# Optimization experiments

Measured on AMD Instinct MI355X. Metric: run time of the kernel, lower is better.

The kernel has to match this reference:

```python
import jax, jax.numpy as jnp
import numpy as np
from jax.scipy.linalg import cho_solve

N = 4096        # num nodes
D = 256         # in_dim == out_dim
NUM_HOPS = 2
R = 32          # subspace_dim
ETA = 0.5
EPS_SUB = 0.5   # eps in coeff = r / (n * eps^2)
LN_EPS = 1e-5


def setup_inputs() -> dict:
    rng = np.random.default_rng(0)
    K = NUM_HOPS + 1
    # sparse-ish binary adjacency mask with self loops
    mask = (rng.random((N, N)) < 0.002).astype(np.float32)
    mask = np.maximum(mask, np.eye(N, dtype=np.float32))
    deg = mask.sum(axis=1, keepdims=True)
    A = (mask / deg).astype(np.float32)          # row-stochastic propagation
    L = (np.eye(N, dtype=np.float32) - A)        # normalized Laplacian
    H = rng.standard_normal((N, D)).astype(np.float32)
    # orthonormal subspace bases per hop, as in __init__ (QR of randn)
    U = np.stack([np.linalg.qr(rng.standard_normal((D, R)))[0][:, :R] for _ in range(K)]).astype(np.float32)
    lambda_laps = np.full((K,), 0.1, dtype=np.float32)
    hop_weights = np.full((K,), 1.0 / K, dtype=np.float32)
    threshold = np.full((D,), 0.05, dtype=np.float32)
    gamma = np.ones((D,), dtype=np.float32)
    beta = np.zeros((D,), dtype=np.float32)
    return {
        "H": jnp.asarray(H), "A": jnp.asarray(A), "adj_mask": jnp.asarray(mask),
        "L": jnp.asarray(L), "U": jnp.asarray(U),
        "lambda_laps": jnp.asarray(lambda_laps), "hop_weights": jnp.asarray(hop_weights),
        "threshold": jnp.asarray(threshold), "gamma": jnp.asarray(gamma), "beta": jnp.asarray(beta),
    }


def reference(H, A, adj_mask, L, U, lambda_laps, hop_weights, threshold, gamma, beta):
    n, d = H.shape
    r = U.shape[-1]
    # multi-hop propagation
    hops = [H]
    Hk = H
    for _ in range(NUM_HOPS):
        Hk = A @ Hk
        hops.append(Hk)
    w = jax.nn.softmax(hop_weights)
    laps = jax.nn.softplus(lambda_laps)
    coeff = r / (n * EPS_SUB ** 2)
    neg = (1.0 - adj_mask) * -1e9
    I_r = jnp.eye(r, dtype=H.dtype)
    agg = jnp.zeros_like(H)        # accumulates grad_k.T, shape [n, d]
    lap_total = jnp.zeros_like(H)
    for k, H_k in enumerate(hops):
        Uk = U[k]                  # [d, r]
        Zk = Uk.T @ H_k.T          # [r, n]
        M = I_r + coeff * (Zk @ Zk.T)              # [r, r], SPD
        Lc = jnp.linalg.cholesky(M)
        M_inv = cho_solve((Lc, True), I_r)         # cholesky_inverse
        MZ = M_inv @ Zk                            # [r, n]
        scores = Zk.T @ MZ + neg                   # [n, n] masked subspace attention
        alpha = jax.nn.softmax(scores, axis=1)
        grad_k = (Uk @ (MZ @ alpha.T)).T           # [n, d]
        agg = agg + w[k] * grad_k
        lap_total = lap_total + laps[k] * (L @ H_k)
    H_half = H + ETA * agg - ETA * lap_total
    # soft-threshold (proj is None since in_dim == out_dim)
    H_out = jnp.sign(H_half) * jax.nn.relu(jnp.abs(H_half) - threshold[None, :])
    H_out = H_out + H              # residual
    mu = H_out.mean(axis=-1, keepdims=True)
    var = H_out.var(axis=-1, keepdims=True)
    H_out = (H_out - mu) / jnp.sqrt(var + LN_EPS) * gamma + beta
    # orthogonality loss over all (k, l) pairs
    K = U.shape[0]
    orth_loss = jnp.asarray(0.0, dtype=H.dtype)
    for k in range(K):
        for l in range(k, K):
            G = U[k].T @ U[l]
            orth_loss = orth_loss + jnp.sum(((G - I_r) if l == k else G) ** 2)
    lap_smooth = jnp.sum(H_out * (L @ H_out))  # trace(H^T L H)
    return H_out, orth_loss, lap_smooth, jax.lax.stop_gradient(w)
```

## Files before the change

### kernel.cpp

```cpp
#include <hip/hip_runtime.h>
#include <math.h>

#define NN 4096
#define DD 256
#define KK 3
#define RR 32
#define MAXNNZ 128

static constexpr float ETA    = 0.5f;
static constexpr float COEFF  = 0.03125f;
static constexpr float LN_EPSF = 1e-5f;

#define OFF_H1   0
#define OFF_H2   (NN*DD)
#define OFF_H3   (2*NN*DD)
#define OFF_Y    (3*NN*DD)
#define OFF_W    (OFF_Y + KK*NN*RR)
#define OFF_P    (OFF_W + KK*NN*RR)
#define OFF_M    (OFF_P + KK*NN*RR)
#define OFF_MINV (OFF_M + KK*RR*RR)
#define OFF_SCAL (OFF_MINV + KK*RR*RR)
#define OFF_NNZ  (OFF_SCAL + 8)
#define OFF_COLS (OFF_NNZ + NN)
#define OFF_VALS (OFF_COLS + NN*MAXNNZ)
#define OFF_PART (OFF_VALS + NN*MAXNNZ)

__global__ void k_prep(const float* __restrict__ hw, const float* __restrict__ ll,
                       float* __restrict__ ws, float* __restrict__ out) {
  int t = threadIdx.x;
  if (t == 0) {
    float m = fmaxf(fmaxf(hw[0], hw[1]), hw[2]);
    float e0 = expf(hw[0]-m), e1 = expf(hw[1]-m), e2 = expf(hw[2]-m);
    float s = e0 + e1 + e2;
    float w0 = e0/s, w1 = e1/s, w2 = e2/s;
    ws[OFF_SCAL+0] = w0; ws[OFF_SCAL+1] = w1; ws[OFF_SCAL+2] = w2;
    for (int k = 0; k < KK; ++k) {
      float x = ll[k];
      ws[OFF_SCAL+3+k] = (x > 20.f) ? x : log1pf(expf(x));
    }
    out[NN*DD + 0] = 0.f;
    out[NN*DD + 2] = w0; out[NN*DD + 3] = w1; out[NN*DD + 4] = w2;
  }
  for (int idx = t; idx < KK*RR*RR; idx += blockDim.x) {
    int rr2 = idx % (RR*RR);
    ws[OFF_M + idx] = ((rr2 / RR) == (rr2 % RR)) ? 1.f : 0.f;
  }
}

__global__ void k_csr(const float* __restrict__ A, int* __restrict__ nnz,
                      int* __restrict__ cols, float* __restrict__ vals) {
  int i = blockIdx.x;
  __shared__ int cnt;
  if (threadIdx.x == 0) cnt = 0;
  __syncthreads();
  const float4* row4 = (const float4*)(A + (size_t)i * NN);
  for (int j0 = 0; j0 < NN/4; j0 += 256) {
    float4 v = row4[j0 + threadIdx.x];
    int jb = (j0 + threadIdx.x) * 4;
    if (v.x != 0.f) { int p = atomicAdd(&cnt,1); if (p<MAXNNZ){cols[i*MAXNNZ+p]=jb+0; vals[i*MAXNNZ+p]=v.x;} }
    if (v.y != 0.f) { int p = atomicAdd(&cnt,1); if (p<MAXNNZ){cols[i*MAXNNZ+p]=jb+1; vals[i*MAXNNZ+p]=v.y;} }
    if (v.z != 0.f) { int p = atomicAdd(&cnt,1); if (p<MAXNNZ){cols[i*MAXNNZ+p]=jb+2; vals[i*MAXNNZ+p]=v.z;} }
    if (v.w != 0.f) { int p = atomicAdd(&cnt,1); if (p<MAXNNZ){cols[i*MAXNNZ+p]=jb+3; vals[i*MAXNNZ+p]=v.w;} }
  }
  __syncthreads();
  int n = cnt < MAXNNZ ? cnt : MAXNNZ;
  int npad = (n + 7) & ~7;
  for (int e = n + threadIdx.x; e < npad; e += 256) {
    cols[i*MAXNNZ + e] = i;
    vals[i*MAXNNZ + e] = 0.f;
  }
  if (threadIdx.x == 0) nnz[i] = n;
}

__global__ void k_spmv(const float* __restrict__ X, float* __restrict__ Y,
                       const int* __restrict__ nnz, const int* __restrict__ cols,
                       const float* __restrict__ vals) {
  int t = threadIdx.x;
  int row = blockIdx.x * 4 + (t >> 6);
  int d4 = (t & 63) * 4;
  int n = nnz[row];
  int npad = (n + 7) & ~7;
  const int* ci = cols + row*MAXNNZ;
  const float* vi = vals + row*MAXNNZ;
  float4 acc = {0.f, 0.f, 0.f, 0.f};
  for (int e0 = 0; e0 < npad; e0 += 8) {
    int4 c0 = *(const int4*)(ci + e0);
    int4 c1 = *(const int4*)(ci + e0 + 4);
    float4 v0 = *(const float4*)(vi + e0);
    float4 v1 = *(const float4*)(vi + e0 + 4);
    float4 x0 = *(const float4*)(X + (size_t)c0.x*DD + d4);
    float4 x1 = *(const float4*)(X + (size_t)c0.y*DD + d4);
    float4 x2 = *(const float4*)(X + (size_t)c0.z*DD + d4);
    float4 x3 = *(const float4*)(X + (size_t)c0.w*DD + d4);
    float4 x4 = *(const float4*)(X + (size_t)c1.x*DD + d4);
    float4 x5 = *(const float4*)(X + (size_t)c1.y*DD + d4);
    float4 x6 = *(const float4*)(X + (size_t)c1.z*DD + d4);
    float4 x7 = *(const float4*)(X + (size_t)c1.w*DD + d4);
    acc.x += v0.x*x0.x + v0.y*x1.x + v0.z*x2.x + v0.w*x3.x + v1.x*x4.x + v1.y*x5.x + v1.z*x6.x + v1.w*x7.x;
    acc.y += v0.x*x0.y + v0.y*x1.y + v0.z*x2.y + v0.w*x3.y + v1.x*x4.y + v1.y*x5.y + v1.z*x6.y + v1.w*x7.y;
    acc.z += v0.x*x0.z + v0.y*x1.z + v0.z*x2.z + v0.w*x3.z + v1.x*x4.z + v1.y*x5.z + v1.z*x6.z + v1.w*x7.z;
    acc.w += v0.x*x0.w + v0.y*x1.w + v0.z*x2.w + v0.w*x3.w + v1.x*x4.w + v1.y*x5.w + v1.z*x6.w + v1.w*x7.w;
  }
  *(float4*)(Y + (size_t)row*DD + d4) = acc;
}

__global__ void k_yproj(const float* __restrict__ H0, const float* __restrict__ Hws,
                        const float* __restrict__ U, float* __restrict__ Y) {
  int k = blockIdx.y;
  const float* Hk = (k == 0) ? H0 : (Hws + (size_t)(k-1)*NN*DD);
  __shared__ float Us[DD*RR];
  __shared__ float Hs[8][DD];
  int t = threadIdx.x;
  for (int idx = t; idx < DD*RR; idx += 256) Us[idx] = U[(size_t)k*DD*RR + idx];
  int row0 = blockIdx.x * 8;
  for (int r = 0; r < 8; ++r) Hs[r][t] = Hk[(size_t)(row0+r)*DD + t];
  __syncthreads();
  int rl = t >> 5, c = t & 31;
  const float4* H4 = (const float4*)Hs[rl];
  float acc = 0.f;
  for (int dd4 = 0; dd4 < DD/4; ++dd4) {
    float4 hv = H4[dd4];
    int b = dd4 * 4 * RR + c;
    acc += hv.x*Us[b] + hv.y*Us[b+RR] + hv.z*Us[b+2*RR] + hv.w*Us[b+3*RR];
  }
  Y[(size_t)k*NN*RR + (size_t)(row0+rl)*RR + c] = acc;
}

__global__ __launch_bounds__(1024) void k_gram(const float* __restrict__ Y, float* __restrict__ M) {
  int k = blockIdx.y;
  __shared__ float Ys[128*RR];
  int t = threadIdx.x;
  const float* Yk = Y + (size_t)k*NN*RR + (size_t)blockIdx.x*128*RR;
  for (int idx = t; idx < 128*RR; idx += 1024) Ys[idx] = Yk[idx];
  __syncthreads();
  int a = t >> 5, b = t & 31;
  float s = 0.f;
  for (int i = 0; i < 128; ++i) s += Ys[i*RR + a] * Ys[i*RR + b];
  atomicAdd(&M[k*RR*RR + a*RR + b], COEFF * s);
}

__global__ __launch_bounds__(1024) void k_cholinv(const float* __restrict__ M, float* __restrict__ Minv) {
  int k = blockIdx.x;
  __shared__ float L[RR][RR+1];
  __shared__ float Li[RR][RR+1];
  int t = threadIdx.x;
  int r = t >> 5, c = t & 31;
  L[r][c] = M[k*RR*RR + r*RR + c];
  Li[r][c] = 0.f;
  __syncthreads();
  for (int j = 0; j < RR; ++j) {
    if (t == j*32 + j) L[j][j] = sqrtf(L[j][j]);
    __syncthreads();
    if (c == j && r > j) L[r][j] /= L[j][j];
    __syncthreads();
    if (r > j && c > j && c <= r) L[r][c] -= L[r][j] * L[c][j];
    __syncthreads();
  }
  if (t < RR) {
    int cc = t;
    Li[cc][cc] = 1.f / L[cc][cc];
    for (int rr2 = cc+1; rr2 < RR; ++rr2) {
      float s = 0.f;
      for (int j = cc; j < rr2; ++j) s += L[rr2][j] * Li[j][cc];
      Li[rr2][cc] = -s / L[rr2][rr2];
    }
  }
  __syncthreads();
  float s = 0.f;
  int j0 = (r > c) ? r : c;
  for (int j = j0; j < RR; ++j) s += Li[j][r] * Li[j][c];
  Minv[k*RR*RR + r*RR + c] = s;
}

__global__ void k_wproj(const float* __restrict__ Y, const float* __restrict__ Minv,
                        float* __restrict__ W) {
  int k = blockIdx.y;
  __shared__ float Ms[RR*RR];
  __shared__ float Ys[8*RR];
  int t = threadIdx.x;
  for (int idx = t; idx < RR*RR; idx += 256) Ms[idx] = Minv[k*RR*RR + idx];
  int row0 = blockIdx.x * 8;
  Ys[t] = Y[(size_t)k*NN*RR + (size_t)row0*RR + t];
  __syncthreads();
  int rl = t >> 5, c = t & 31;
  float acc = 0.f;
  for (int a = 0; a < RR; ++a) acc += Ys[rl*RR + a] * Ms[a*RR + c];
  W[(size_t)k*NN*RR + (size_t)(row0+rl)*RR + c] = acc;
}

__global__ void k_attn(const float* __restrict__ Y, const float* __restrict__ W,
                       float* __restrict__ P, const int* __restrict__ nnz,
                       const int* __restrict__ cols) {
  int i = blockIdx.x;
  int t = threadIdx.x;
  int half = t >> 5, lane = t & 31;
  int n = nnz[i];
  int npad = (n + 7) & ~7;
  const int* ci = cols + i*MAXNNZ;
  __shared__ float sc[MAXNNZ];
  __shared__ float outp[2][RR];
  for (int k = 0; k < KK; ++k) {
    const float* Yk = Y + (size_t)k*NN*RR;
    const float* Wk = W + (size_t)k*NN*RR;
    float yv = Yk[(size_t)i*RR + lane];
    for (int e0 = 0; e0 < npad; e0 += 8) {
      #pragma unroll
      for (int u = 0; u < 4; ++u) {
        int e = e0 + 2*u + half;
        float p = yv * Wk[(size_t)ci[e]*RR + lane];
        #pragma unroll
        for (int o = 16; o > 0; o >>= 1) p += __shfl_down(p, o, 32);
        if (lane == 0) sc[e] = (e < n) ? p : -1e30f;
      }
    }
    __syncthreads();
    float s0 = (t < npad) ? sc[t] : -1e30f;
    float s1 = (t+64 < npad) ? sc[t+64] : -1e30f;
    float m = fmaxf(s0, s1);
    #pragma unroll
    for (int o = 32; o > 0; o >>= 1) m = fmaxf(m, __shfl_xor(m, o, 64));
    float ev0 = (t < npad) ? expf(s0 - m) : 0.f;
    float ev1 = (t+64 < npad) ? expf(s1 - m) : 0.f;
    if (t < npad) sc[t] = ev0;
    if (t+64 < npad) sc[t+64] = ev1;
    float l = ev0 + ev1;
    #pragma unroll
    for (int o = 32; o > 0; o >>= 1) l += __shfl_xor(l, o, 64);
    float linv = 1.f / l;
    __syncthreads();
    float acc = 0.f;
    for (int e0 = 0; e0 < npad; e0 += 8) {
      #pragma unroll
      for (int u = 0; u < 4; ++u) {
        int e = e0 + 2*u + half;
        acc += sc[e] * Wk[(size_t)ci[e]*RR + lane];
      }
    }
    outp[half][lane] = acc;
    __syncthreads();
    if (t < RR) P[(size_t)k*NN*RR + (size_t)i*RR + t] = (outp[0][t] + outp[1][t]) * linv;
    __syncthreads();
  }
}

__global__ void k_epi(const float* __restrict__ H0, const float* __restrict__ ws,
                      const float* __restrict__ U, const float* __restrict__ thr,
                      const float* __restrict__ gma, const float* __restrict__ bta,
                      float* __restrict__ out) {
  __shared__ float Us[DD][RR+1];
  __shared__ float Ps[8][KK*RR];
  int t = threadIdx.x;
  int ty = t >> 5, tx = t & 31;
  int row0 = blockIdx.x * 8;
  const float* P    = ws + OFF_P;
  const float* scal = ws + OFF_SCAL;
  for (int idx = t; idx < 8*KK*RR; idx += 256) {
    int rl = idx / (KK*RR), kr = idx % (KK*RR);
    int k = kr / RR, rr2 = kr % RR;
    Ps[rl][kr] = P[(size_t)k*NN*RR + (size_t)(row0+rl)*RR + rr2];
  }
  float lp0 = scal[3], lp1 = scal[4], lp2 = scal[5];
  float gacc[8];
  #pragma unroll
  for (int j = 0; j < 8; ++j) gacc[j] = 0.f;
  for (int k = 0; k < KK; ++k) {
    __syncthreads();
    for (int idx = t; idx < DD*RR; idx += 256) Us[idx >> 5][idx & 31] = U[(size_t)k*DD*RR + idx];
    __syncthreads();
    float wk = scal[k];
    #pragma unroll
    for (int j = 0; j < 8; ++j) {
      int d = tx + 32*j;
      float s = 0.f;
      #pragma unroll
      for (int rr2 = 0; rr2 < RR; ++rr2) s += Ps[ty][k*RR + rr2] * Us[d][rr2];
      gacc[j] += wk * s;
    }
  }
  int i = row0 + ty;
  const float* H1 = ws + OFF_H1;
  const float* H2 = ws + OFF_H2;
  const float* H3 = ws + OFF_H3;
  float v[8]; float sum = 0.f, sumsq = 0.f;
  #pragma unroll
  for (int j = 0; j < 8; ++j) {
    int d = tx + 32*j;
    size_t idx = (size_t)i*DD + d;
    float h0 = H0[idx], h1 = H1[idx], h2 = H2[idx], h3 = H3[idx];
    float lap = lp0*(h0-h1) + lp1*(h1-h2) + lp2*(h2-h3);
    float hf = h0 + ETA*gacc[j] - ETA*lap;
    float a = fabsf(hf) - thr[d];
    float sft = (a > 0.f) ? copysignf(a, hf) : 0.f;
    float x = sft + h0;
    v[j] = x; sum += x; sumsq += x*x;
  }
  #pragma unroll
  for (int o = 16; o > 0; o >>= 1) {
    sum   += __shfl_xor(sum, o, 32);
    sumsq += __shfl_xor(sumsq, o, 32);
  }
  float mu  = sum * (1.f/DD);
  float var = sumsq * (1.f/DD) - mu*mu;
  float inv = rsqrtf(var + LN_EPSF);
  #pragma unroll
  for (int j = 0; j < 8; ++j) {
    int d = tx + 32*j;
    out[(size_t)i*DD + d] = (v[j] - mu) * inv * gma[d] + bta[d];
  }
}

__global__ void k_lapsm(const float* __restrict__ Hout, const int* __restrict__ nnz,
                        const int* __restrict__ cols, const float* __restrict__ vals,
                        float* __restrict__ partial) {
  int t = threadIdx.x;
  int row = blockIdx.x * 4 + (t >> 6);
  int d4 = (t & 63) * 4;
  int n = nnz[row];
  int npad = (n + 7) & ~7;
  const int* ci = cols + row*MAXNNZ;
  const float* vi = vals + row*MAXNNZ;
  float4 acc = {0.f, 0.f, 0.f, 0.f};
  for (int e0 = 0; e0 < npad; e0 += 8) {
    int4 c0 = *(const int4*)(ci + e0);
    int4 c1 = *(const int4*)(ci + e0 + 4);
    float4 v0 = *(const float4*)(vi + e0);
    float4 v1 = *(const float4*)(vi + e0 + 4);
    float4 x0 = *(const float4*)(Hout + (size_t)c0.x*DD + d4);
    float4 x1 = *(const float4*)(Hout + (size_t)c0.y*DD + d4);
    float4 x2 = *(const float4*)(Hout + (size_t)c0.z*DD + d4);
    float4 x3 = *(const float4*)(Hout + (size_t)c0.w*DD + d4);
    float4 x4 = *(const float4*)(Hout + (size_t)c1.x*DD + d4);
    float4 x5 = *(const float4*)(Hout + (size_t)c1.y*DD + d4);
    float4 x6 = *(const float4*)(Hout + (size_t)c1.z*DD + d4);
    float4 x7 = *(const float4*)(Hout + (size_t)c1.w*DD + d4);
    acc.x += v0.x*x0.x + v0.y*x1.x + v0.z*x2.x + v0.w*x3.x + v1.x*x4.x + v1.y*x5.x + v1.z*x6.x + v1.w*x7.x;
    acc.y += v0.x*x0.y + v0.y*x1.y + v0.z*x2.y + v0.w*x3.y + v1.x*x4.y + v1.y*x5.y + v1.z*x6.y + v1.w*x7.y;
    acc.z += v0.x*x0.z + v0.y*x1.z + v0.z*x2.z + v0.w*x3.z + v1.x*x4.z + v1.y*x5.z + v1.z*x6.z + v1.w*x7.z;
    acc.w += v0.x*x0.w + v0.y*x1.w + v0.z*x2.w + v0.w*x3.w + v1.x*x4.w + v1.y*x5.w + v1.z*x6.w + v1.w*x7.w;
  }
  float4 h = *(const float4*)(Hout + (size_t)row*DD + d4);
  float part = h.x*(h.x-acc.x) + h.y*(h.y-acc.y) + h.z*(h.z-acc.z) + h.w*(h.w-acc.w);
  #pragma unroll
  for (int o = 32; o > 0; o >>= 1) part += __shfl_xor(part, o, 64);
  __shared__ float red[4];
  if ((t & 63) == 0) red[t >> 6] = part;
  __syncthreads();
  if (t == 0) partial[blockIdx.x] = red[0] + red[1] + red[2] + red[3];
}

__global__ void k_red(const float* __restrict__ partial, float* __restrict__ out) {
  int t = threadIdx.x;
  float4 p = *(const float4*)(partial + t*4);
  float s = p.x + p.y + p.z + p.w;
  #pragma unroll
  for (int o = 32; o > 0; o >>= 1) s += __shfl_xor(s, o, 64);
  __shared__ float red[4];
  if ((t & 63) == 0) red[t >> 6] = s;
  __syncthreads();
  if (t == 0) out[0] = red[0] + red[1] + red[2] + red[3];
}

__global__ __launch_bounds__(1024) void k_orth(const float* __restrict__ U, float* __restrict__ out) {
  int p = blockIdx.x;
  int k = (p < 3) ? 0 : ((p < 5) ? 1 : 2);
  int l = (p < 3) ? p : ((p < 5) ? p - 2 : 2);
  int t = threadIdx.x;
  int a = t >> 5, b = t & 31;
  float s = 0.f;
  for (int dd = 0; dd < DD; ++dd)
    s += U[(size_t)k*DD*RR + dd*RR + a] * U[(size_t)l*DD*RR + dd*RR + b];
  if (k == l && a == b) s -= 1.f;
  float sq = s * s;
  __shared__ float red[1024];
  red[t] = sq;
  __syncthreads();
  for (int st = 512; st > 0; st >>= 1) {
    if (t < st) red[t] += red[t + st];
    __syncthreads();
  }
  if (t == 0) atomicAdd(out, red[0]);
}

extern "C" void kernel_launch(void* const* d_in, const int* in_sizes, int n_in,
                              void* d_out, int out_size, void* d_ws, size_t ws_size,
                              hipStream_t stream) {
  const float* H   = (const float*)d_in[0];
  const float* A   = (const float*)d_in[1];
  const float* U   = (const float*)d_in[4];
  const float* ll  = (const float*)d_in[5];
  const float* hw  = (const float*)d_in[6];
  const float* thr = (const float*)d_in[7];
  const float* gma = (const float*)d_in[8];
  const float* bta = (const float*)d_in[9];
  float* out = (float*)d_out;
  float* ws  = (float*)d_ws;
  int* nnz   = (int*)(ws + OFF_NNZ);
  int* cols  = (int*)(ws + OFF_COLS);
  float* vals = ws + OFF_VALS;

  k_prep<<<1, 64, 0, stream>>>(hw, ll, ws, out);
  k_csr<<<NN, 256, 0, stream>>>(A, nnz, cols, vals);
  k_spmv<<<NN/4, 256, 0, stream>>>(H,            ws + OFF_H1, nnz, cols, vals);
  k_spmv<<<NN/4, 256, 0, stream>>>(ws + OFF_H1,  ws + OFF_H2, nnz, cols, vals);
  k_spmv<<<NN/4, 256, 0, stream>>>(ws + OFF_H2,  ws + OFF_H3, nnz, cols, vals);
  dim3 g512(NN/8, KK);
  k_yproj<<<g512, 256, 0, stream>>>(H, ws + OFF_H1, U, ws + OFF_Y);
  dim3 g32(NN/128, KK);
  k_gram<<<g32, 1024, 0, stream>>>(ws + OFF_Y, ws + OFF_M);
  k_cholinv<<<KK, 1024, 0, stream>>>(ws + OFF_M, ws + OFF_MINV);
  k_wproj<<<g512, 256, 0, stream>>>(ws + OFF_Y, ws + OFF_MINV, ws + OFF_W);
  k_attn<<<NN, 64, 0, stream>>>(ws + OFF_Y, ws + OFF_W, ws + OFF_P, nnz, cols);
  k_epi<<<NN/8, 256, 0, stream>>>(H, ws, U, thr, gma, bta, out);
  k_lapsm<<<NN/4, 256, 0, stream>>>(out, nnz, cols, vals, ws + OFF_PART);
  k_red<<<1, 256, 0, stream>>>(ws + OFF_PART, out + NN*DD + 1);
  k_orth<<<6, 1024, 0, stream>>>(U, out + NN*DD + 0);
}
```

Measured before the change: 327.2 us.

## Fuse subspace projection into SpMV, merge prep/orth, use Gauss-Jordan, parallelize attention

Folds the Y = H_k U_k projection into the propagation SpMV kernels, taking H_0 from the self-loop neighbor and H_1/H_2 from the freshly computed rows, which removes the separate yproj pass over the hop matrices. It merges the orthogonality-loss kernel into the prep kernel and adds its result in the final reduction, replacing an atomic and one launch. Cholesky plus triangular inverse is replaced by Gauss-Jordan elimination, which needs fewer barriers. Attention is split across hops via a 2D grid, with per-edge dot products done per thread. The own-row capture relies on self loops being present in the adjacency, and Gauss-Jordan without pivoting is less numerically robust than Cholesky.

```diff
diff --git a/kernel.cpp b/kernel.cpp
--- a/kernel.cpp
+++ b/kernel.cpp
@@ -24,27 +24,49 @@
 #define OFF_COLS (OFF_NNZ + NN)
 #define OFF_VALS (OFF_COLS + NN*MAXNNZ)
 #define OFF_PART (OFF_VALS + NN*MAXNNZ)
-
-__global__ void k_prep(const float* __restrict__ hw, const float* __restrict__ ll,
+#define OFF_ORTH (OFF_PART + NN/4)
+
+__global__ __launch_bounds__(1024) void k_prep_orth(const float* __restrict__ hw,
+                       const float* __restrict__ ll, const float* __restrict__ U,
                        float* __restrict__ ws, float* __restrict__ out) {
-  int t = threadIdx.x;
-  if (t == 0) {
-    float m = fmaxf(fmaxf(hw[0], hw[1]), hw[2]);
-    float e0 = expf(hw[0]-m), e1 = expf(hw[1]-m), e2 = expf(hw[2]-m);
-    float s = e0 + e1 + e2;
-    float w0 = e0/s, w1 = e1/s, w2 = e2/s;
-    ws[OFF_SCAL+0] = w0; ws[OFF_SCAL+1] = w1; ws[OFF_SCAL+2] = w2;
-    for (int k = 0; k < KK; ++k) {
-      float x = ll[k];
-      ws[OFF_SCAL+3+k] = (x > 20.f) ? x : log1pf(expf(x));
+  int b = blockIdx.x;
+  int t = threadIdx.x;
+  if (b == 6) {
+    if (t == 0) {
+      float m = fmaxf(fmaxf(hw[0], hw[1]), hw[2]);
+      float e0 = expf(hw[0]-m), e1 = expf(hw[1]-m), e2 = expf(hw[2]-m);
+      float s = e0 + e1 + e2;
+      float w0 = e0/s, w1 = e1/s, w2 = e2/s;
+      ws[OFF_SCAL+0] = w0; ws[OFF_SCAL+1] = w1; ws[OFF_SCAL+2] = w2;
+      for (int k = 0; k < KK; ++k) {
+        float x = ll[k];
+        ws[OFF_SCAL+3+k] = (x > 20.f) ? x : log1pf(expf(x));
+      }
+      out[NN*DD + 2] = w0; out[NN*DD + 3] = w1; out[NN*DD + 4] = w2;
     }
-    out[NN*DD + 0] = 0.f;
-    out[NN*DD + 2] = w0; out[NN*DD + 3] = w1; out[NN*DD + 4] = w2;
-  }
-  for (int idx = t; idx < KK*RR*RR; idx += blockDim.x) {
-    int rr2 = idx % (RR*RR);
-    ws[OFF_M + idx] = ((rr2 / RR) == (rr2 % RR)) ? 1.f : 0.f;
-  }
+    for (int idx = t; idx < KK*RR*RR; idx += 1024) {
+      int rr2 = idx % (RR*RR);
+      ws[OFF_M + idx] = ((rr2 / RR) == (rr2 % RR)) ? 1.f : 0.f;
+    }
+    return;
+  }
+  int p = b;
+  int k = (p < 3) ? 0 : ((p < 5) ? 1 : 2);
+  int l = (p < 3) ? p : ((p < 5) ? p - 2 : 2);
+  int a = t >> 5, bb = t & 31;
+  float s = 0.f;
+  for (int dd = 0; dd < DD; ++dd)
+    s += U[(size_t)k*DD*RR + dd*RR + a] * U[(size_t)l*DD*RR + dd*RR + bb];
+  if (k == l && a == bb) s -= 1.f;
+  float sq = s * s;
+  __shared__ float red[1024];
+  red[t] = sq;
+  __syncthreads();
+  for (int st = 512; st > 0; st >>= 1) {
+    if (t < st) red[t] += red[t + st];
+    __syncthreads();
+  }
+  if (t == 0) ws[OFF_ORTH + p] = red[0];
 }
 
 __global__ void k_csr(const float* __restrict__ A, int* __restrict__ nnz,
@@ -72,17 +94,21 @@
   if (threadIdx.x == 0) nnz[i] = n;
 }
 
-__global__ void k_spmv(const float* __restrict__ X, float* __restrict__ Y,
-                       const int* __restrict__ nnz, const int* __restrict__ cols,
-                       const float* __restrict__ vals) {
-  int t = threadIdx.x;
-  int row = blockIdx.x * 4 + (t >> 6);
-  int d4 = (t & 63) * 4;
+__global__ void k_spmvy(const float* __restrict__ X, float* __restrict__ Hout,
+                        const int* __restrict__ nnz, const int* __restrict__ cols,
+                        const float* __restrict__ vals,
+                        const float* __restrict__ Uo, float* __restrict__ Yo,
+                        const float* __restrict__ Un, float* __restrict__ Yn) {
+  int t = threadIdx.x;
+  int r = t >> 6, lane = t & 63;
+  int row = blockIdx.x * 4 + r;
+  int d4 = lane * 4;
   int n = nnz[row];
   int npad = (n + 7) & ~7;
   const int* ci = cols + row*MAXNNZ;
   const float* vi = vals + row*MAXNNZ;
   float4 acc = {0.f, 0.f, 0.f, 0.f};
+  float4 own = {0.f, 0.f, 0.f, 0.f};
   for (int e0 = 0; e0 < npad; e0 += 8) {
     int4 c0 = *(const int4*)(ci + e0);
     int4 c1 = *(const int4*)(ci + e0 + 4);
@@ -96,34 +122,40 @@
     float4 x5 = *(const float4*)(X + (size_t)c1.y*DD + d4);
     float4 x6 = *(const float4*)(X + (size_t)c1.z*DD + d4);
     float4 x7 = *(const float4*)(X + (size_t)c1.w*DD + d4);
+    if (c0.x == row) own = x0;
+    if (c0.y == row) own = x1;
+    if (c0.z == row) own = x2;
+    if (c0.w == row) own = x3;
+    if (c1.x == row) own = x4;
+    if (c1.y == row) own = x5;
+    if (c1.z == row) own = x6;
+    if (c1.w == row) own = x7;
     acc.x += v0.x*x0.x + v0.y*x1.x + v0.z*x2.x + v0.w*x3.x + v1.x*x4.x + v1.y*x5.x + v1.z*x6.x + v1.w*x7.x;
     acc.y += v0.x*x0.y + v0.y*x1.y + v0.z*x2.y + v0.w*x3.y + v1.x*x4.y + v1.y*x5.y + v1.z*x6.y + v1.w*x7.y;
     acc.z += v0.x*x0.z + v0.y*x1.z + v0.z*x2.z + v0.w*x3.z + v1.x*x4.z + v1.y*x5.z + v1.z*x6.z + v1.w*x7.z;
     acc.w += v0.x*x0.w + v0.y*x1.w + v0.z*x2.w + v0.w*x3.w + v1.x*x4.w + v1.y*x5.w + v1.z*x6.w + v1.w*x7.w;
   }
-  *(float4*)(Y + (size_t)row*DD + d4) = acc;
-}
-
-__global__ void k_yproj(const float* __restrict__ H0, const float* __restrict__ Hws,
-                        const float* __restrict__ U, float* __restrict__ Y) {
-  int k = blockIdx.y;
-  const float* Hk = (k == 0) ? H0 : (Hws + (size_t)(k-1)*NN*DD);
-  __shared__ float Us[DD*RR];
-  __shared__ float Hs[8][DD];
-  int t = threadIdx.x;
-  for (int idx = t; idx < DD*RR; idx += 256) Us[idx] = U[(size_t)k*DD*RR + idx];
-  int row0 = blockIdx.x * 8;
-  for (int r = 0; r < 8; ++r) Hs[r][t] = Hk[(size_t)(row0+r)*DD + t];
-  __syncthreads();
-  int rl = t >> 5, c = t & 31;
-  const float4* H4 = (const float4*)Hs[rl];
-  float acc = 0.f;
-  for (int dd4 = 0; dd4 < DD/4; ++dd4) {
-    float4 hv = H4[dd4];
-    int b = dd4 * 4 * RR + c;
-    acc += hv.x*Us[b] + hv.y*Us[b+RR] + hv.z*Us[b+2*RR] + hv.w*Us[b+3*RR];
-  }
-  Y[(size_t)k*NN*RR + (size_t)(row0+rl)*RR + c] = acc;
+  *(float4*)(Hout + (size_t)row*DD + d4) = acc;
+  if (!Uo && !Un) return;
+  __shared__ float Hs[4][2][DD];
+  *(float4*)&Hs[r][0][d4] = own;
+  *(float4*)&Hs[r][1][d4] = acc;
+  __syncthreads();
+  int c = lane & 31, h = lane >> 5;
+  if (Uo) {
+    float part = 0.f;
+    #pragma unroll 8
+    for (int d = h*128; d < h*128 + 128; ++d) part += Hs[r][0][d] * Uo[d*RR + c];
+    part += __shfl_xor(part, 32, 64);
+    if (h == 0) Yo[(size_t)row*RR + c] = part;
+  }
+  if (Un) {
+    float part = 0.f;
+    #pragma unroll 8
+    for (int d = h*128; d < h*128 + 128; ++d) part += Hs[r][1][d] * Un[d*RR + c];
+    part += __shfl_xor(part, 32, 64);
+    if (h == 0) Yn[(size_t)row*RR + c] = part;
+  }
 }
 
 __global__ __launch_bounds__(1024) void k_gram(const float* __restrict__ Y, float* __restrict__ M) {
@@ -139,37 +171,35 @@
   atomicAdd(&M[k*RR*RR + a*RR + b], COEFF * s);
 }
 
-__global__ __launch_bounds__(1024) void k_cholinv(const float* __restrict__ M, float* __restrict__ Minv) {
+__global__ __launch_bounds__(256) void k_gj(const float* __restrict__ M, float* __restrict__ Minv) {
   int k = blockIdx.x;
-  __shared__ float L[RR][RR+1];
-  __shared__ float Li[RR][RR+1];
-  int t = threadIdx.x;
-  int r = t >> 5, c = t & 31;
-  L[r][c] = M[k*RR*RR + r*RR + c];
-  Li[r][c] = 0.f;
-  __syncthreads();
+  __shared__ float B[RR][2*RR];
+  int t = threadIdx.x;
+  for (int idx = t; idx < RR*2*RR; idx += 256) {
+    int r = idx >> 6, c = idx & 63;
+    B[r][c] = (c < RR) ? M[k*RR*RR + r*RR + c] : ((c - RR == r) ? 1.f : 0.f);
+  }
+  __syncthreads();
+  int c = t & 63, r0 = t >> 6;
   for (int j = 0; j < RR; ++j) {
-    if (t == j*32 + j) L[j][j] = sqrtf(L[j][j]);
+    float bjc = B[j][c];
+    float pinv = 1.f / B[j][j];
+    float f[8];
+    #pragma unroll
+    for (int q = 0; q < 8; ++q) f[q] = B[r0 + 4*q][j];
     __syncthreads();
-    if (c == j && r > j) L[r][j] /= L[j][j];
+    float pb = pinv * bjc;
+    #pragma unroll
+    for (int q = 0; q < 8; ++q) {
+      int r = r0 + 4*q;
+      B[r][c] = (r == j) ? pb : (B[r][c] - f[q] * pb);
+    }
     __syncthreads();
-    if (r > j && c > j && c <= r) L[r][c] -= L[r][j] * L[c][j];
-    __syncthreads();
-  }
-  if (t < RR) {
-    int cc = t;
-    Li[cc][cc] = 1.f / L[cc][cc];
-    for (int rr2 = cc+1; rr2 < RR; ++rr2) {
-      float s = 0.f;
-      for (int j = cc; j < rr2; ++j) s += L[rr2][j] * Li[j][cc];
-      Li[rr2][cc] = -s / L[rr2][rr2];
-    }
-  }
-  __syncthreads();
-  float s = 0.f;
-  int j0 = (r > c) ? r : c;
-  for (int j = j0; j < RR; ++j) s += Li[j][r] * Li[j][c];
-  Minv[k*RR*RR + r*RR + c] = s;
+  }
+  for (int idx = t; idx < RR*RR; idx += 256) {
+    int r = idx >> 5, cc = idx & 31;
+    Minv[k*RR*RR + r*RR + cc] = B[r][RR + cc];
+  }
 }
 
 __global__ void k_wproj(const float* __restrict__ Y, const float* __restrict__ Minv,
@@ -191,56 +221,45 @@
 __global__ void k_attn(const float* __restrict__ Y, const float* __restrict__ W,
                        float* __restrict__ P, const int* __restrict__ nnz,
                        const int* __restrict__ cols) {
-  int i = blockIdx.x;
-  int t = threadIdx.x;
-  int half = t >> 5, lane = t & 31;
+  int i = blockIdx.x, k = blockIdx.y;
+  int t = threadIdx.x;
+  const float* Yk = Y + (size_t)k*NN*RR;
+  const float* Wk = W + (size_t)k*NN*RR;
   int n = nnz[i];
   int npad = (n + 7) & ~7;
   const int* ci = cols + i*MAXNNZ;
+  __shared__ float Ys[RR];
   __shared__ float sc[MAXNNZ];
-  __shared__ float outp[2][RR];
-  for (int k = 0; k < KK; ++k) {
-    const float* Yk = Y + (size_t)k*NN*RR;
-    const float* Wk = W + (size_t)k*NN*RR;
-    float yv = Yk[(size_t)i*RR + lane];
-    for (int e0 = 0; e0 < npad; e0 += 8) {
-      #pragma unroll
-      for (int u = 0; u < 4; ++u) {
-        int e = e0 + 2*u + half;
-        float p = yv * Wk[(size_t)ci[e]*RR + lane];
-        #pragma unroll
-        for (int o = 16; o > 0; o >>= 1) p += __shfl_down(p, o, 32);
-        if (lane == 0) sc[e] = (e < n) ? p : -1e30f;
-      }
+  if (t < RR) Ys[t] = Yk[(size_t)i*RR + t];
+  sc[t] = -1e30f; sc[t+64] = -1e30f;
+  __syncthreads();
+  for (int e = t; e < npad; e += 64) {
+    const float4* wr = (const float4*)(Wk + (size_t)ci[e]*RR);
+    float s = 0.f;
+    #pragma unroll
+    for (int q = 0; q < 8; ++q) {
+      float4 wv = wr[q];
+      s += wv.x*Ys[4*q] + wv.y*Ys[4*q+1] + wv.z*Ys[4*q+2] + wv.w*Ys[4*q+3];
     }
-    __syncthreads();
-    float s0 = (t < npad) ? sc[t] : -1e30f;
-    float s1 = (t+64 < npad) ? sc[t+64] : -1e30f;
-    float m = fmaxf(s0, s1);
-    #pragma unroll
-    for (int o = 32; o > 0; o >>= 1) m = fmaxf(m, __shfl_xor(m, o, 64));
-    float ev0 = (t < npad) ? expf(s0 - m) : 0.f;
-    float ev1 = (t+64 < npad) ? expf(s1 - m) : 0.f;
-    if (t < npad) sc[t] = ev0;
-    if (t+64 < npad) sc[t+64] = ev1;
-    float l = ev0 + ev1;
-    #pragma unroll
-    for (int o = 32; o > 0; o >>= 1) l += __shfl_xor(l, o, 64);
-    float linv = 1.f / l;
-    __syncthreads();
-    float acc = 0.f;
-    for (int e0 = 0; e0 < npad; e0 += 8) {
-      #pragma unroll
-      for (int u = 0; u < 4; ++u) {
-        int e = e0 + 2*u + half;
-        acc += sc[e] * Wk[(size_t)ci[e]*RR + lane];
-      }
-    }
-    outp[half][lane] = acc;
-    __syncthreads();
-    if (t < RR) P[(size_t)k*NN*RR + (size_t)i*RR + t] = (outp[0][t] + outp[1][t]) * linv;
-    __syncthreads();
-  }
+    sc[e] = (e < n) ? s : -1e30f;
+  }
+  __syncthreads();
+  float s0 = sc[t], s1 = sc[t+64];
+  float m = fmaxf(s0, s1);
+  #pragma unroll
+  for (int o = 32; o > 0; o >>= 1) m = fmaxf(m, __shfl_xor(m, o, 64));
+  float e0v = expf(s0 - m), e1v = expf(s1 - m);
+  sc[t] = e0v; sc[t+64] = e1v;
+  float l = e0v + e1v;
+  #pragma unroll
+  for (int o = 32; o > 0; o >>= 1) l += __shfl_xor(l, o, 64);
+  float linv = 1.f / l;
+  __syncthreads();
+  int c = t & 31, h = t >> 5;
+  float acc = 0.f;
+  for (int e = h; e < npad; e += 2) acc += sc[e] * Wk[(size_t)ci[e]*RR + c];
+  acc += __shfl_xor(acc, 32, 64);
+  if (t < RR) P[(size_t)k*NN*RR + (size_t)i*RR + t] = acc * linv;
 }
 
 __global__ void k_epi(const float* __restrict__ H0, const float* __restrict__ ws,
@@ -348,7 +367,8 @@
   if (t == 0) partial[blockIdx.x] = red[0] + red[1] + red[2] + red[3];
 }
 
-__global__ void k_red(const float* __restrict__ partial, float* __restrict__ out) {
+__global__ void k_red(const float* __restrict__ ws, float* __restrict__ out) {
+  const float* partial = ws + OFF_PART;
   int t = threadIdx.x;
   float4 p = *(const float4*)(partial + t*4);
   float s = p.x + p.y + p.z + p.w;
@@ -357,28 +377,11 @@
   __shared__ float red[4];
   if ((t & 63) == 0) red[t >> 6] = s;
   __syncthreads();
-  if (t == 0) out[0] = red[0] + red[1] + red[2] + red[3];
-}
-
-__global__ __launch_bounds__(1024) void k_orth(const float* __restrict__ U, float* __restrict__ out) {
-  int p = blockIdx.x;
-  int k = (p < 3) ? 0 : ((p < 5) ? 1 : 2);
-  int l = (p < 3) ? p : ((p < 5) ? p - 2 : 2);
-  int t = threadIdx.x;
-  int a = t >> 5, b = t & 31;
-  float s = 0.f;
-  for (int dd = 0; dd < DD; ++dd)
-    s += U[(size_t)k*DD*RR + dd*RR + a] * U[(size_t)l*DD*RR + dd*RR + b];
-  if (k == l && a == b) s -= 1.f;
-  float sq = s * s;
-  __shared__ float red[1024];
-  red[t] = sq;
-  __syncthreads();
-  for (int st = 512; st > 0; st >>= 1) {
-    if (t < st) red[t] += red[t + st];
-    __syncthreads();
-  }
-  if (t == 0) atomicAdd(out, red[0]);
+  if (t == 0) {
+    out[1] = red[0] + red[1] + red[2] + red[3];
+    const float* op = ws + OFF_ORTH;
+    out[0] = op[0] + op[1] + op[2] + op[3] + op[4] + op[5];
+  }
 }
 
 extern "C" void kernel_launch(void* const* d_in, const int* in_sizes, int n_in,
@@ -397,21 +400,24 @@
   int* nnz   = (int*)(ws + OFF_NNZ);
   int* cols  = (int*)(ws + OFF_COLS);
   float* vals = ws + OFF_VALS;
-
-  k_prep<<<1, 64, 0, stream>>>(hw, ll, ws, out);
+  float* Y = ws + OFF_Y;
+
+  k_prep_orth<<<7, 1024, 0, stream>>>(hw, ll, U, ws, out);
   k_csr<<<NN, 256, 0, stream>>>(A, nnz, cols, vals);
-  k_spmv<<<NN/4, 256, 0, stream>>>(H,            ws + OFF_H1, nnz, cols, vals);
-  k_spmv<<<NN/4, 256, 0, stream>>>(ws + OFF_H1,  ws + OFF_H2, nnz, cols, vals);
-  k_spmv<<<NN/4, 256, 0, stream>>>(ws + OFF_H2,  ws + OFF_H3, nnz, cols, vals);
+  k_spmvy<<<NN/4, 256, 0, stream>>>(H, ws + OFF_H1, nnz, cols, vals,
+                                    U, Y, U + (size_t)DD*RR, Y + (size_t)NN*RR);
+  k_spmvy<<<NN/4, 256, 0, stream>>>(ws + OFF_H1, ws + OFF_H2, nnz, cols, vals,
+                                    nullptr, nullptr, U + (size_t)2*DD*RR, Y + (size_t)2*NN*RR);
+  k_spmvy<<<NN/4, 256, 0, stream>>>(ws + OFF_H2, ws + OFF_H3, nnz, cols, vals,
+                                    nullptr, nullptr, nullptr, nullptr);
+  dim3 g32(NN/128, KK);
+  k_gram<<<g32, 1024, 0, stream>>>(Y, ws + OFF_M);
+  k_gj<<<KK, 256, 0, stream>>>(ws + OFF_M, ws + OFF_MINV);
   dim3 g512(NN/8, KK);
-  k_yproj<<<g512, 256, 0, stream>>>(H, ws + OFF_H1, U, ws + OFF_Y);
-  dim3 g32(NN/128, KK);
-  k_gram<<<g32, 1024, 0, stream>>>(ws + OFF_Y, ws + OFF_M);
-  k_cholinv<<<KK, 1024, 0, stream>>>(ws + OFF_M, ws + OFF_MINV);
-  k_wproj<<<g512, 256, 0, stream>>>(ws + OFF_Y, ws + OFF_MINV, ws + OFF_W);
-  k_attn<<<NN, 64, 0, stream>>>(ws + OFF_Y, ws + OFF_W, ws + OFF_P, nnz, cols);
+  k_wproj<<<g512, 256, 0, stream>>>(Y, ws + OFF_MINV, ws + OFF_W);
+  dim3 gattn(NN, KK);
+  k_attn<<<gattn, 64, 0, stream>>>(Y, ws + OFF_W, ws + OFF_P, nnz, cols);
   k_epi<<<NN/8, 256, 0, stream>>>(H, ws, U, thr, gma, bta, out);
   k_lapsm<<<NN/4, 256, 0, stream>>>(out, nnz, cols, vals, ws + OFF_PART);
-  k_red<<<1, 256, 0, stream>>>(ws + OFF_PART, out + NN*DD + 1);
-  k_orth<<<6, 1024, 0, stream>>>(U, out + NN*DD + 0);
-}
+  k_red<<<1, 256, 0, stream>>>(ws, out + NN*DD);
+}
```

After: 300.7 us. 1.09x faster.
